# Performance work log

Hardware: AMD Instinct MI355X
Metric: run time of the kernel (lower is better)

The kernel has to match this reference:

```python
import jax, jax.numpy as jnp
import numpy as np

B, N, D, R, NUM_HEADS, S = 8, 512, 256, 6, 3, 1000


def setup_inputs() -> dict:
    key = jax.random.key(0)
    ks = jax.random.split(key, 12)
    init = lambda k, shape: jax.random.normal(k, shape, jnp.float32) * 0.02
    return {
        "symbol_ids": jax.random.randint(ks[0], (B, N), 0, S),
        "positions": jax.random.normal(ks[1], (B, N, 2), jnp.float32),
        "sym_table": init(ks[2], (S, D)),
        "layer_table": init(ks[3], (S, D)),      # layer-0 interpretation embedding
        "rel_W": init(ks[4], (R, D, D)),          # per-relation Linear weights (in,out)
        "rel_b": init(ks[5], (R, D)),
        "h1_W": init(ks[6], (NUM_HEADS, D, D)),   # interpretation head Linear1
        "h1_b": init(ks[7], (NUM_HEADS, D)),
        "h2_W": init(ks[8], (NUM_HEADS, D)),      # interpretation head Linear2 (D->1)
        "h2_b": init(ks[9], (NUM_HEADS,)),
        "out_W": init(ks[10], (D, D)),
        "out_b": init(ks[11], (D,)),
    }


def _relation_type(dx, dy):
    # Vectorized version of PositionalGrammar._get_relation_type (if/elif chain)
    return jnp.select(
        [dy > 0.5, dy < -0.5, dx < -0.5, dx > 0.5,
         (jnp.abs(dx) < 0.3) & (jnp.abs(dy) < 0.3)],
        [0, 1, 2, 3, 4], 5)


def _positional_grammar(symbols, positions, rel_W, rel_b):
    # transformed[b,j] = symbols[b,j] + sum_{i!=j} (symbols[b,i] @ W_r(i,j) + b_r(i,j))
    dx = positions[:, None, :, 0] - positions[:, :, None, 0]  # [b,i,j]
    dy = positions[:, None, :, 1] - positions[:, :, None, 1]
    rel = _relation_type(dx, dy)                               # [b,i,j] int
    n = symbols.shape[1]
    not_self = ~jnp.eye(n, dtype=bool)
    # one-hot relation mask, self-pairs excluded: [b,i,j,r]
    M = ((rel[..., None] == jnp.arange(R)) & not_self[None, :, :, None]).astype(symbols.dtype)
    T = jnp.einsum('bid,rde->brie', symbols, rel_W)            # per-relation transform of sources
    contrib = jnp.einsum('bijr,brie->bje', M, T)               # scatter-add over sources i
    bias = jnp.einsum('bijr,re->bje', M, rel_b)                # per-pair bias accumulation
    return symbols + contrib + bias


def reference(symbol_ids, positions, sym_table, layer_table, rel_W, rel_b,
              h1_W, h1_b, h2_W, h2_b, out_W, out_b):
    # SymbolEmbedding (calendar_pos=None path; layer=0)
    symbols = sym_table[symbol_ids] + layer_table[symbol_ids]  # [B,N,D]
    # PositionalGrammar
    symbols = _positional_grammar(symbols, positions, rel_W, rel_b)
    # LayeredInterpretation: 3 heads of Linear-GELU-Linear(D->1)
    h = jax.nn.gelu(jnp.einsum('bnd,rde->brne', symbols, h1_W)
                    + h1_b[None, :, None, :], approximate=False)
    interp = jnp.einsum('brne,re->brn', h, h2_W) + h2_b[None, :, None]  # [B,3,N]
    # output projection
    output = symbols @ out_W + out_b
    return (output,
            interp[:, 0, :, None],   # exoteric  [B,N,1]
            interp[:, 1, :, None],   # esoteric
            interp[:, 2, :, None],   # sacred
            symbols)
```

## Files before the change

kernel.cpp:

```cpp
#include <hip/hip_runtime.h>
#include <hip/hip_bf16.h>
#include <math.h>

#define BB 8
#define NN 512
#define DD 256
#define BNT 4096

typedef __attribute__((ext_vector_type(8))) short short8;
typedef __attribute__((ext_vector_type(4))) float f32x4;

#define OFF_S0B   0u
#define OFF_TT    524288u
#define OFF_WCT   6815744u
#define OFF_WBT   7012352u
#define OFF_BB    7143424u
#define OFF_REL   7144448u

#define OUT0_OFF   0u
#define INTERP_OFF 1048576u
#define SYM_OFF    1060864u

__device__ __forceinline__ float gelu_exact(float x) {
    return 0.5f * x * (1.0f + erff(x * 0.70710678118654752f));
}

__device__ __forceinline__ ushort f2bf(float x) {
    __hip_bfloat16 h = __float2bfloat16(x);
    union { __hip_bfloat16 b; ushort u; } cv;
    cv.b = h;
    return cv.u;
}

__device__ __forceinline__ int rel_of(float dx, float dy) {
    int r = (fabsf(dx) < 0.3f && fabsf(dy) < 0.3f) ? 4 : 5;
    r = (dx >  0.5f) ? 3 : r;
    r = (dx < -0.5f) ? 2 : r;
    r = (dy < -0.5f) ? 1 : r;
    r = (dy >  0.5f) ? 0 : r;
    return r;
}

#define TILE_IDS()                                             \
    const int lane = tid & 63, w = tid >> 6;                   \
    const int wm = w >> 1, wn = w & 1;                         \
    const int quad = lane >> 4, l15 = lane & 15;               \
    const int sm = tid >> 2, sq = tid & 3;

#define MFMA_STEP(Abuf, Bbuf)                                                \
    {                                                                        \
        short8 af[2], bfr[2];                                                \
        _Pragma("unroll")                                                    \
        for (int mt = 0; mt < 2; mt++)                                       \
            af[mt] = *(const short8*)&(Abuf)[(quad * 64 + wm * 32 + mt * 16 + l15) * 8]; \
        _Pragma("unroll")                                                    \
        for (int nt = 0; nt < 2; nt++)                                       \
            bfr[nt] = *(const short8*)&(Bbuf)[(quad * 64 + wn * 32 + nt * 16 + l15) * 8]; \
        _Pragma("unroll")                                                    \
        for (int mt = 0; mt < 2; mt++)                                       \
            _Pragma("unroll")                                                \
            for (int nt = 0; nt < 2; nt++)                                   \
                acc[mt][nt] = __builtin_amdgcn_mfma_f32_16x16x32_bf16(       \
                    af[mt], bfr[nt], acc[mt][nt], 0, 0, 0);                  \
    }

#define ACC_INIT()                                             \
    f32x4 acc[2][2];                                           \
    _Pragma("unroll") for (int mt = 0; mt < 2; mt++)           \
    _Pragma("unroll") for (int nt = 0; nt < 2; nt++)           \
        acc[mt][nt] = (f32x4){0.f, 0.f, 0.f, 0.f};

__global__ __launch_bounds__(256) void front_kernel(
    const int* __restrict__ ids, const float* __restrict__ positions,
    const float* __restrict__ symt, const float* __restrict__ layt,
    const float* __restrict__ relW, const float* __restrict__ h1W,
    const float* __restrict__ outW, const float* __restrict__ h1b,
    const float* __restrict__ outb, const float* __restrict__ h2b,
    ushort* __restrict__ WcT, ushort* __restrict__ WbT,
    float* __restrict__ bbig, float* __restrict__ outI,
    float* __restrict__ symOut, ushort* __restrict__ s0b,
    unsigned char* __restrict__ rel)
{
    __shared__ float px[NN], py[NN];
    int blk = blockIdx.x, tid = threadIdx.x;
    if (blk < 1536) {
        int idx = blk * 256 + tid;
        {
            int e = idx / 1536, k = idx - e * 1536;
            int r = k >> 8, d = k & 255;
            WcT[idx] = f2bf(relW[(r * DD + d) * DD + e]);
        }
        if (idx < 262144) {
            int c = idx >> 8, d = idx & 255;
            float v;
            if (c < 768) { int r = c >> 8, e = c & 255; v = h1W[(r * DD + d) * DD + e]; }
            else         { v = outW[d * DD + (c - 768)]; }
            WbT[idx] = f2bf(v);
        }
        if (idx < 3 * BNT) outI[idx] = h2b[idx >> 12];
        if (idx < 1024) bbig[idx] = (idx < 768) ? h1b[idx] : outb[idx - 768];
    } else if (blk < 5632) {
        int row = blk - 1536;
        int id = ids[row];
        float v = symt[id * DD + tid] + layt[id * DD + tid];
        symOut[(size_t)row * DD + tid] = v;
        s0b[(size_t)row * DD + tid] = f2bf(v);
    } else {
        int blk2 = blk - 5632;
        int b = blk2 >> 6;
        int j0 = (blk2 & 63) << 3;
        int jl = tid >> 5, sub = tid & 31;
        for (int i = tid; i < NN; i += 256) {
            float2 p = ((const float2*)positions)[b * NN + i];
            px[i] = p.x; py[i] = p.y;
        }
        __syncthreads();
        int j = j0 + jl;
        float xj = px[j], yj = py[j];
        union { unsigned char u8[16]; uint4 v; } codes;
#pragma unroll
        for (int t = 0; t < 16; t++) {
            int i = sub * 16 + t;
            int r = rel_of(xj - px[i], yj - py[i]);
            r = (i == j) ? 6 : r;
            codes.u8[t] = (unsigned char)r;
        }
        *(uint4*)&rel[((size_t)(b * NN + j)) * NN + sub * 16] = codes.v;
    }
}

__global__ __launch_bounds__(256) void gemmT_kernel(
    const ushort* __restrict__ WcT, const ushort* __restrict__ s0b,
    const float* __restrict__ relb, ushort* __restrict__ TT)
{
    __shared__ ushort Als[2][2048], Bls[2][2048];
    int tid = threadIdx.x;
    int b = blockIdx.z;
    int rowM0 = blockIdx.y * 64;
    int col0 = blockIdx.x * 64;
    int r = rowM0 >> 8, e0 = rowM0 & 255;
    TILE_IDS();
    ACC_INIT();
    const ushort* gA = WcT + (size_t)(e0 + sm) * 1536 + r * 256 + sq * 8;
    const ushort* gB = s0b + ((size_t)(b * NN) + col0 + sm) * DD + sq * 8;
    const int lo = (sq * 64 + sm) * 8;

    *(uint4*)&Als[0][lo] = *(const uint4*)gA;
    *(uint4*)&Bls[0][lo] = *(const uint4*)gB;
#pragma unroll
    for (int i = 0; i < 8; i++) {
        __syncthreads();
        uint4 av2, bv2;
        if (i < 7) {
            av2 = *(const uint4*)(gA + (i + 1) * 32);
            bv2 = *(const uint4*)(gB + (i + 1) * 32);
        }
        MFMA_STEP(Als[i & 1], Bls[i & 1]);
        if (i < 7) {
            *(uint4*)&Als[(i + 1) & 1][lo] = av2;
            *(uint4*)&Bls[(i + 1) & 1][lo] = bv2;
        }
    }
#pragma unroll
    for (int mt = 0; mt < 2; mt++)
#pragma unroll
        for (int nt = 0; nt < 2; nt++)
#pragma unroll
            for (int v = 0; v < 4; v++) {
                int e = e0 + wm * 32 + mt * 16 + quad * 4 + v;
                int i = col0 + wn * 32 + nt * 16 + l15;
                TT[((size_t)(b * DD) + e) * 3072 + r * 512 + i] =
                    f2bf(acc[mt][nt][v] + relb[r * DD + e]);
            }
}

__global__ __launch_bounds__(256) void agg_gemm(
    const unsigned char* __restrict__ rel, const ushort* __restrict__ TT,
    float* __restrict__ symOut)
{
    __shared__ ushort Als[2][2048], Bls[2][2048];
    int tid = threadIdx.x;
    int z = blockIdx.z;
    int b = z / 3, rg = z - b * 3;
    int row0 = blockIdx.y * 64, col0 = blockIdx.x * 64;
    TILE_IDS();
    ACC_INIT();
    const unsigned char* gC = rel + ((size_t)(b * NN + row0 + sm)) * NN;
    const ushort* gB = TT + ((size_t)(b * DD) + col0 + sm) * 3072 + rg * 1024 + sq * 8;
    const int lo = (sq * 64 + sm) * 8;

#define AGG_LOADS(i, cw, bv)                                        \
    cw = *(const uint2*)(gC + (((i) * 32 + sq * 8) & 511));         \
    bv = *(const uint4*)(gB + (i) * 32);

#define AGG_STAGE(i, cw, bv, buf)                                   \
    {                                                               \
        int rr_ = 2 * rg + (((i) * 32) >> 9);                       \
        union alignas(16) { ushort u[8]; uint4 v; } am;             \
        _Pragma("unroll")                                           \
        for (int t = 0; t < 8; t++) {                               \
            unsigned int word = (t < 4) ? cw.x : cw.y;              \
            unsigned int code = (word >> (8 * (t & 3))) & 255u;     \
            am.u[t] = (code == (unsigned)rr_) ? 0x3F80 : 0;         \
        }                                                           \
        *(uint4*)&Als[buf][lo] = am.v;                              \
        *(uint4*)&Bls[buf][lo] = bv;                                \
    }

    uint2 cw0; uint4 bv0;
    AGG_LOADS(0, cw0, bv0);
    AGG_STAGE(0, cw0, bv0, 0);
    for (int i = 0; i < 32; i++) {
        __syncthreads();
        uint2 cw2; uint4 bv2;
        if (i < 31) { AGG_LOADS(i + 1, cw2, bv2); }
        MFMA_STEP(Als[i & 1], Bls[i & 1]);
        if (i < 31) { AGG_STAGE(i + 1, cw2, bv2, (i + 1) & 1); }
    }
#undef AGG_LOADS
#undef AGG_STAGE
#pragma unroll
    for (int mt = 0; mt < 2; mt++)
#pragma unroll
        for (int nt = 0; nt < 2; nt++)
#pragma unroll
            for (int v = 0; v < 4; v++) {
                int j = row0 + wm * 32 + mt * 16 + quad * 4 + v;
                int e = col0 + wn * 32 + nt * 16 + l15;
                atomicAdd(&symOut[((size_t)(b * NN) + j) * DD + e], acc[mt][nt][v]);
            }
}

__global__ __launch_bounds__(256) void gemm2_kernel(
    const float* __restrict__ symOut, const ushort* __restrict__ WbT,
    const float* __restrict__ bbig, const float* __restrict__ h2W,
    float* __restrict__ out0, float* __restrict__ outI)
{
    __shared__ ushort Als[2][2048], Bls[2][2048];
    int tid = threadIdx.x;
    int row0 = blockIdx.y * 64, col0 = blockIdx.x * 64;
    TILE_IDS();
    ACC_INIT();
    const float*  gA = symOut + (size_t)(row0 + sm) * DD + sq * 8;
    const ushort* gB = WbT    + (size_t)(col0 + sm) * DD + sq * 8;
    const int lo = (sq * 64 + sm) * 8;

#define G2_LOADS(i, a0, a1, bv)                                     \
    a0 = *(const float4*)(gA + (i) * 32);                           \
    a1 = *(const float4*)(gA + (i) * 32 + 4);                       \
    bv = *(const uint4*)(gB + (i) * 32);

#define G2_STAGE(a0, a1, bv, buf)                                   \
    {                                                               \
        union alignas(16) { ushort u[8]; uint4 v; } am;             \
        am.u[0] = f2bf(a0.x); am.u[1] = f2bf(a0.y);                 \
        am.u[2] = f2bf(a0.z); am.u[3] = f2bf(a0.w);                 \
        am.u[4] = f2bf(a1.x); am.u[5] = f2bf(a1.y);                 \
        am.u[6] = f2bf(a1.z); am.u[7] = f2bf(a1.w);                 \
        *(uint4*)&Als[buf][lo] = am.v;                              \
        *(uint4*)&Bls[buf][lo] = bv;                                \
    }

    float4 a0, a1; uint4 bv;
    G2_LOADS(0, a0, a1, bv);
    G2_STAGE(a0, a1, bv, 0);
#pragma unroll
    for (int i = 0; i < 8; i++) {
        __syncthreads();
        float4 a0n, a1n; uint4 bvn;
        if (i < 7) { G2_LOADS(i + 1, a0n, a1n, bvn); }
        MFMA_STEP(Als[i & 1], Bls[i & 1]);
        if (i < 7) { G2_STAGE(a0n, a1n, bvn, (i + 1) & 1); }
    }
#undef G2_LOADS
#undef G2_STAGE
    if (col0 >= 768) {
#pragma unroll
        for (int nt = 0; nt < 2; nt++) {
            int c = col0 + wn * 32 + nt * 16 + l15;
            float bb = bbig[c];
#pragma unroll
            for (int mt = 0; mt < 2; mt++)
#pragma unroll
                for (int v = 0; v < 4; v++) {
                    int row = row0 + wm * 32 + mt * 16 + quad * 4 + v;
                    out0[(size_t)row * DD + (c - 768)] = acc[mt][nt][v] + bb;
                }
        }
    } else {
        int head = col0 >> 8;
        float part[2][4];
#pragma unroll
        for (int mt = 0; mt < 2; mt++)
#pragma unroll
            for (int v = 0; v < 4; v++) part[mt][v] = 0.f;
#pragma unroll
        for (int nt = 0; nt < 2; nt++) {
            int c = col0 + wn * 32 + nt * 16 + l15;
            float bb = bbig[c];
            float w2 = h2W[c];
#pragma unroll
            for (int mt = 0; mt < 2; mt++)
#pragma unroll
                for (int v = 0; v < 4; v++)
                    part[mt][v] += gelu_exact(acc[mt][nt][v] + bb) * w2;
        }
#pragma unroll
        for (int mt = 0; mt < 2; mt++)
#pragma unroll
            for (int v = 0; v < 4; v++) {
                float p = part[mt][v];
                p += __shfl_xor(p, 1); p += __shfl_xor(p, 2);
                p += __shfl_xor(p, 4); p += __shfl_xor(p, 8);
                if (l15 == 0) {
                    int row = row0 + wm * 32 + mt * 16 + quad * 4 + v;
                    atomicAdd(&outI[head * BNT + row], p);
                }
            }
    }
}

extern "C" void kernel_launch(void* const* d_in, const int* in_sizes, int n_in,
                              void* d_out, int out_size, void* d_ws, size_t ws_size,
                              hipStream_t stream)
{
    const int*   ids  = (const int*)d_in[0];
    const float* pos  = (const float*)d_in[1];
    const float* symt = (const float*)d_in[2];
    const float* layt = (const float*)d_in[3];
    const float* relW = (const float*)d_in[4];
    const float* relb = (const float*)d_in[5];
    const float* h1W  = (const float*)d_in[6];
    const float* h1b  = (const float*)d_in[7];
    const float* h2W  = (const float*)d_in[8];
    const float* h2b  = (const float*)d_in[9];
    const float* outW = (const float*)d_in[10];
    const float* outb = (const float*)d_in[11];
    float* out = (float*)d_out;
    float* ws  = (float*)d_ws;

    ushort* s0b  = (ushort*)(ws + OFF_S0B);
    ushort* TT   = (ushort*)(ws + OFF_TT);
    ushort* WcT  = (ushort*)(ws + OFF_WCT);
    ushort* WbT  = (ushort*)(ws + OFF_WBT);
    float*  bbig = ws + OFF_BB;
    unsigned char* rel = (unsigned char*)(ws + OFF_REL);

    front_kernel<<<6144, 256, 0, stream>>>(ids, pos, symt, layt, relW, h1W, outW,
                                           h1b, outb, h2b, WcT, WbT, bbig,
                                           out + INTERP_OFF, out + SYM_OFF, s0b, rel);
    gemmT_kernel<<<dim3(8, 24, 8), 256, 0, stream>>>(WcT, s0b, relb, TT);
    agg_gemm<<<dim3(4, 8, 24), 256, 0, stream>>>(rel, TT, out + SYM_OFF);
    gemm2_kernel<<<dim3(16, 64), 256, 0, stream>>>(out + SYM_OFF, WbT,
                                                   bbig, h2W,
                                                   out + OUT0_OFF, out + INTERP_OFF);
}
```

Baseline: 140.9 us.

## Drop LDS staging in GEMMs, load MFMA fragments directly from global

All three GEMM kernels stop staging tiles through double-buffered shared memory with __syncthreads. Each wave now loads its MFMA operand fragments straight from global memory, and the aggregation GEMM builds its one-hot operand in registers. Separately, the embedding gather in front_kernel is vectorised to float4, with 4 rows per block, which halves its grid. This removes barriers and LDS traffic but loses cross-wave reuse, so each wave re-reads its operands from cache, and latency hiding now depends on occupancy.

```diff
diff --git a/kernel.cpp b/kernel.cpp
--- a/kernel.cpp
+++ b/kernel.cpp
@@ -41,34 +41,41 @@
     return r;
 }
 
-#define TILE_IDS()                                             \
+__device__ __forceinline__ short8 pack_bf8(float4 x, float4 y) {
+    union { ushort u[8]; short8 v; } o;
+    o.u[0] = f2bf(x.x); o.u[1] = f2bf(x.y); o.u[2] = f2bf(x.z); o.u[3] = f2bf(x.w);
+    o.u[4] = f2bf(y.x); o.u[5] = f2bf(y.y); o.u[6] = f2bf(y.z); o.u[7] = f2bf(y.w);
+    return o.v;
+}
+
+__device__ __forceinline__ short8 onehot8(uint2 cw, unsigned rr) {
+    union { ushort u[8]; short8 v; } o;
+    unsigned m = rr * 0x01010101u;
+    unsigned x = cw.x ^ m, y = cw.y ^ m;
+#pragma unroll
+    for (int t = 0; t < 4; t++) {
+        o.u[t]     = (((x >> (8 * t)) & 255u) == 0u) ? 0x3F80 : 0;
+        o.u[t + 4] = (((y >> (8 * t)) & 255u) == 0u) ? 0x3F80 : 0;
+    }
+    return o.v;
+}
+
+#define WAVE_IDS()                                             \
     const int lane = tid & 63, w = tid >> 6;                   \
     const int wm = w >> 1, wn = w & 1;                         \
-    const int quad = lane >> 4, l15 = lane & 15;               \
-    const int sm = tid >> 2, sq = tid & 3;
-
-#define MFMA_STEP(Abuf, Bbuf)                                                \
-    {                                                                        \
-        short8 af[2], bfr[2];                                                \
-        _Pragma("unroll")                                                    \
-        for (int mt = 0; mt < 2; mt++)                                       \
-            af[mt] = *(const short8*)&(Abuf)[(quad * 64 + wm * 32 + mt * 16 + l15) * 8]; \
-        _Pragma("unroll")                                                    \
-        for (int nt = 0; nt < 2; nt++)                                       \
-            bfr[nt] = *(const short8*)&(Bbuf)[(quad * 64 + wn * 32 + nt * 16 + l15) * 8]; \
-        _Pragma("unroll")                                                    \
-        for (int mt = 0; mt < 2; mt++)                                       \
-            _Pragma("unroll")                                                \
-            for (int nt = 0; nt < 2; nt++)                                   \
-                acc[mt][nt] = __builtin_amdgcn_mfma_f32_16x16x32_bf16(       \
-                    af[mt], bfr[nt], acc[mt][nt], 0, 0, 0);                  \
-    }
+    const int quad = lane >> 4, l15 = lane & 15;
 
 #define ACC_INIT()                                             \
     f32x4 acc[2][2];                                           \
     _Pragma("unroll") for (int mt = 0; mt < 2; mt++)           \
     _Pragma("unroll") for (int nt = 0; nt < 2; nt++)           \
         acc[mt][nt] = (f32x4){0.f, 0.f, 0.f, 0.f};
+
+#define MFMA4(a0, a1, b0, b1)                                                     \
+    acc[0][0] = __builtin_amdgcn_mfma_f32_16x16x32_bf16(a0, b0, acc[0][0], 0, 0, 0); \
+    acc[0][1] = __builtin_amdgcn_mfma_f32_16x16x32_bf16(a0, b1, acc[0][1], 0, 0, 0); \
+    acc[1][0] = __builtin_amdgcn_mfma_f32_16x16x32_bf16(a1, b0, acc[1][0], 0, 0, 0); \
+    acc[1][1] = __builtin_amdgcn_mfma_f32_16x16x32_bf16(a1, b1, acc[1][1], 0, 0, 0);
 
 __global__ __launch_bounds__(256) void front_kernel(
     const int* __restrict__ ids, const float* __restrict__ positions,
@@ -99,14 +106,19 @@
         }
         if (idx < 3 * BNT) outI[idx] = h2b[idx >> 12];
         if (idx < 1024) bbig[idx] = (idx < 768) ? h1b[idx] : outb[idx - 768];
-    } else if (blk < 5632) {
-        int row = blk - 1536;
+    } else if (blk < 2560) {
+        int row = (blk - 1536) * 4 + (tid >> 6);
+        int d = (tid & 63) * 4;
         int id = ids[row];
-        float v = symt[id * DD + tid] + layt[id * DD + tid];
-        symOut[(size_t)row * DD + tid] = v;
-        s0b[(size_t)row * DD + tid] = f2bf(v);
+        float4 a = *(const float4*)&symt[(size_t)id * DD + d];
+        float4 c = *(const float4*)&layt[(size_t)id * DD + d];
+        float4 v = {a.x + c.x, a.y + c.y, a.z + c.z, a.w + c.w};
+        *(float4*)&symOut[(size_t)row * DD + d] = v;
+        union { ushort u[4]; uint2 q; } p;
+        p.u[0] = f2bf(v.x); p.u[1] = f2bf(v.y); p.u[2] = f2bf(v.z); p.u[3] = f2bf(v.w);
+        *(uint2*)&s0b[(size_t)row * DD + d] = p.q;
     } else {
-        int blk2 = blk - 5632;
+        int blk2 = blk - 2560;
         int b = blk2 >> 6;
         int j0 = (blk2 & 63) << 3;
         int jl = tid >> 5, sub = tid & 31;
@@ -133,33 +145,24 @@
     const ushort* __restrict__ WcT, const ushort* __restrict__ s0b,
     const float* __restrict__ relb, ushort* __restrict__ TT)
 {
-    __shared__ ushort Als[2][2048], Bls[2][2048];
     int tid = threadIdx.x;
     int b = blockIdx.z;
     int rowM0 = blockIdx.y * 64;
     int col0 = blockIdx.x * 64;
     int r = rowM0 >> 8, e0 = rowM0 & 255;
-    TILE_IDS();
+    WAVE_IDS();
     ACC_INIT();
-    const ushort* gA = WcT + (size_t)(e0 + sm) * 1536 + r * 256 + sq * 8;
-    const ushort* gB = s0b + ((size_t)(b * NN) + col0 + sm) * DD + sq * 8;
-    const int lo = (sq * 64 + sm) * 8;
-
-    *(uint4*)&Als[0][lo] = *(const uint4*)gA;
-    *(uint4*)&Bls[0][lo] = *(const uint4*)gB;
-#pragma unroll
-    for (int i = 0; i < 8; i++) {
-        __syncthreads();
-        uint4 av2, bv2;
-        if (i < 7) {
-            av2 = *(const uint4*)(gA + (i + 1) * 32);
-            bv2 = *(const uint4*)(gB + (i + 1) * 32);
-        }
-        MFMA_STEP(Als[i & 1], Bls[i & 1]);
-        if (i < 7) {
-            *(uint4*)&Als[(i + 1) & 1][lo] = av2;
-            *(uint4*)&Bls[(i + 1) & 1][lo] = bv2;
-        }
+    const ushort* gA0 = WcT + (size_t)(e0 + wm * 32 + l15) * 1536 + r * 256 + quad * 8;
+    const ushort* gA1 = gA0 + 16 * 1536;
+    const ushort* gB0 = s0b + ((size_t)(b * NN) + col0 + wn * 32 + l15) * DD + quad * 8;
+    const ushort* gB1 = gB0 + 16 * DD;
+#pragma unroll
+    for (int s = 0; s < 8; s++) {
+        short8 a0 = *(const short8*)(gA0 + s * 32);
+        short8 a1 = *(const short8*)(gA1 + s * 32);
+        short8 b0 = *(const short8*)(gB0 + s * 32);
+        short8 b1 = *(const short8*)(gB1 + s * 32);
+        MFMA4(a0, a1, b0, b1);
     }
 #pragma unroll
     for (int mt = 0; mt < 2; mt++)
@@ -178,47 +181,29 @@
     const unsigned char* __restrict__ rel, const ushort* __restrict__ TT,
     float* __restrict__ symOut)
 {
-    __shared__ ushort Als[2][2048], Bls[2][2048];
     int tid = threadIdx.x;
     int z = blockIdx.z;
     int b = z / 3, rg = z - b * 3;
     int row0 = blockIdx.y * 64, col0 = blockIdx.x * 64;
-    TILE_IDS();
+    WAVE_IDS();
     ACC_INIT();
-    const unsigned char* gC = rel + ((size_t)(b * NN + row0 + sm)) * NN;
-    const ushort* gB = TT + ((size_t)(b * DD) + col0 + sm) * 3072 + rg * 1024 + sq * 8;
-    const int lo = (sq * 64 + sm) * 8;
-
-#define AGG_LOADS(i, cw, bv)                                        \
-    cw = *(const uint2*)(gC + (((i) * 32 + sq * 8) & 511));         \
-    bv = *(const uint4*)(gB + (i) * 32);
-
-#define AGG_STAGE(i, cw, bv, buf)                                   \
-    {                                                               \
-        int rr_ = 2 * rg + (((i) * 32) >> 9);                       \
-        union alignas(16) { ushort u[8]; uint4 v; } am;             \
-        _Pragma("unroll")                                           \
-        for (int t = 0; t < 8; t++) {                               \
-            unsigned int word = (t < 4) ? cw.x : cw.y;              \
-            unsigned int code = (word >> (8 * (t & 3))) & 255u;     \
-            am.u[t] = (code == (unsigned)rr_) ? 0x3F80 : 0;         \
-        }                                                           \
-        *(uint4*)&Als[buf][lo] = am.v;                              \
-        *(uint4*)&Bls[buf][lo] = bv;                                \
-    }
-
-    uint2 cw0; uint4 bv0;
-    AGG_LOADS(0, cw0, bv0);
-    AGG_STAGE(0, cw0, bv0, 0);
-    for (int i = 0; i < 32; i++) {
-        __syncthreads();
-        uint2 cw2; uint4 bv2;
-        if (i < 31) { AGG_LOADS(i + 1, cw2, bv2); }
-        MFMA_STEP(Als[i & 1], Bls[i & 1]);
-        if (i < 31) { AGG_STAGE(i + 1, cw2, bv2, (i + 1) & 1); }
-    }
-#undef AGG_LOADS
-#undef AGG_STAGE
+    const unsigned char* gC0 = rel + ((size_t)(b * NN) + row0 + wm * 32 + l15) * NN + quad * 8;
+    const unsigned char* gC1 = gC0 + 16 * NN;
+    const ushort* gB0 = TT + ((size_t)(b * DD) + col0 + wn * 32 + l15) * 3072
+                        + rg * 1024 + quad * 8;
+    const ushort* gB1 = gB0 + 16 * 3072;
+#pragma unroll 8
+    for (int s = 0; s < 32; s++) {
+        unsigned rr = 2u * rg + (unsigned)(s >> 4);
+        int io = (s & 15) * 32;
+        uint2 c0 = *(const uint2*)(gC0 + io);
+        uint2 c1 = *(const uint2*)(gC1 + io);
+        short8 a0 = onehot8(c0, rr);
+        short8 a1 = onehot8(c1, rr);
+        short8 b0 = *(const short8*)(gB0 + s * 32);
+        short8 b1 = *(const short8*)(gB1 + s * 32);
+        MFMA4(a0, a1, b0, b1);
+    }
 #pragma unroll
     for (int mt = 0; mt < 2; mt++)
 #pragma unroll
@@ -236,44 +221,26 @@
     const float* __restrict__ bbig, const float* __restrict__ h2W,
     float* __restrict__ out0, float* __restrict__ outI)
 {
-    __shared__ ushort Als[2][2048], Bls[2][2048];
     int tid = threadIdx.x;
     int row0 = blockIdx.y * 64, col0 = blockIdx.x * 64;
-    TILE_IDS();
+    WAVE_IDS();
     ACC_INIT();
-    const float*  gA = symOut + (size_t)(row0 + sm) * DD + sq * 8;
-    const ushort* gB = WbT    + (size_t)(col0 + sm) * DD + sq * 8;
-    const int lo = (sq * 64 + sm) * 8;
-
-#define G2_LOADS(i, a0, a1, bv)                                     \
-    a0 = *(const float4*)(gA + (i) * 32);                           \
-    a1 = *(const float4*)(gA + (i) * 32 + 4);                       \
-    bv = *(const uint4*)(gB + (i) * 32);
-
-#define G2_STAGE(a0, a1, bv, buf)                                   \
-    {                                                               \
-        union alignas(16) { ushort u[8]; uint4 v; } am;             \
-        am.u[0] = f2bf(a0.x); am.u[1] = f2bf(a0.y);                 \
-        am.u[2] = f2bf(a0.z); am.u[3] = f2bf(a0.w);                 \
-        am.u[4] = f2bf(a1.x); am.u[5] = f2bf(a1.y);                 \
-        am.u[6] = f2bf(a1.z); am.u[7] = f2bf(a1.w);                 \
-        *(uint4*)&Als[buf][lo] = am.v;                              \
-        *(uint4*)&Bls[buf][lo] = bv;                                \
-    }
-
-    float4 a0, a1; uint4 bv;
-    G2_LOADS(0, a0, a1, bv);
-    G2_STAGE(a0, a1, bv, 0);
-#pragma unroll
-    for (int i = 0; i < 8; i++) {
-        __syncthreads();
-        float4 a0n, a1n; uint4 bvn;
-        if (i < 7) { G2_LOADS(i + 1, a0n, a1n, bvn); }
-        MFMA_STEP(Als[i & 1], Bls[i & 1]);
-        if (i < 7) { G2_STAGE(a0n, a1n, bvn, (i + 1) & 1); }
-    }
-#undef G2_LOADS
-#undef G2_STAGE
+    const float*  gA0 = symOut + (size_t)(row0 + wm * 32 + l15) * DD + quad * 8;
+    const float*  gA1 = gA0 + 16 * DD;
+    const ushort* gB0 = WbT + (size_t)(col0 + wn * 32 + l15) * DD + quad * 8;
+    const ushort* gB1 = gB0 + 16 * DD;
+#pragma unroll
+    for (int s = 0; s < 8; s++) {
+        float4 x0 = *(const float4*)(gA0 + s * 32);
+        float4 y0 = *(const float4*)(gA0 + s * 32 + 4);
+        float4 x1 = *(const float4*)(gA1 + s * 32);
+        float4 y1 = *(const float4*)(gA1 + s * 32 + 4);
+        short8 a0 = pack_bf8(x0, y0);
+        short8 a1 = pack_bf8(x1, y1);
+        short8 b0 = *(const short8*)(gB0 + s * 32);
+        short8 b1 = *(const short8*)(gB1 + s * 32);
+        MFMA4(a0, a1, b0, b1);
+    }
     if (col0 >= 768) {
 #pragma unroll
         for (int nt = 0; nt < 2; nt++) {
@@ -346,7 +313,7 @@
     float*  bbig = ws + OFF_BB;
     unsigned char* rel = (unsigned char*)(ws + OFF_REL);
 
-    front_kernel<<<6144, 256, 0, stream>>>(ids, pos, symt, layt, relW, h1W, outW,
+    front_kernel<<<3072, 256, 0, stream>>>(ids, pos, symt, layt, relW, h1W, outW,
                                            h1b, outb, h2b, WcT, WbT, bbig,
                                            out + INTERP_OFF, out + SYM_OFF, s0b, rel);
     gemmT_kernel<<<dim3(8, 24, 8), 256, 0, stream>>>(WcT, s0b, relb, TT);
```

Measured after the change: 186.2 us. 32.2% more time.
